# Kernel optimization log

Hardware: AMD Instinct MI355X
Metric: run time of the kernel (lower is better)

The kernel has to match this reference:

```python
import jax, jax.numpy as jnp
import numpy as np

UNITS = 128000
NEGATIVES = 8192
N = 8192
C = 1024


def _log_uniform_expected_count(ids, num_sampled, range_max):
    # log-uniform (Zipfian) sampler: P(c) = (log(c+2)-log(c+1))/log(range_max+1)
    idf = ids.astype(jnp.float32)
    p = (jnp.log(idf + 2.0) - jnp.log(idf + 1.0)) / jnp.log(jnp.float32(range_max + 1.0))
    # unique sampling expected count: E = -expm1(num_sampled * log1p(-p))
    return -jnp.expm1(jnp.float32(num_sampled) * jnp.log1p(-p))


def setup_inputs() -> dict:
    key = jax.random.key(0)
    k1, k2, k3, k4, k5 = jax.random.split(key, 5)
    inputs = jax.random.normal(k1, (N, C), dtype=jnp.float32)
    targets = jax.random.randint(k2, (N,), 0, UNITS, dtype=jnp.int32)
    sampled = jax.random.randint(k3, (NEGATIVES,), 0, UNITS, dtype=jnp.int32)
    kernel = jax.random.normal(k4, (UNITS, C), dtype=jnp.float32) * 0.02
    bias = jax.random.normal(k5, (UNITS,), dtype=jnp.float32) * 0.01
    return {"inputs": inputs, "targets": targets, "sampled": sampled, "kernel": kernel, "bias": bias}


def reference(inputs, targets, sampled, kernel, bias):
    # --- tf.nn.sampled_softmax_loss with log_uniform_candidate_sampler ---
    # gather true class rows: [N, C], [N]
    true_w = kernel[targets]
    true_b = bias[targets]
    # gather sampled class rows: [S, C], [S]
    samp_w = kernel[sampled]
    samp_b = bias[sampled]
    # true logits: [N]
    true_logits = jnp.einsum('nc,nc->n', inputs, true_w) + true_b
    # sampled logits: [N, S]
    samp_logits = jnp.einsum('nc,sc->ns', inputs, samp_w) + samp_b[None, :]
    # remove accidental hits (sampled id == true label)
    acc = sampled[None, :] == targets[:, None]
    samp_logits = jnp.where(acc, samp_logits - 1e9, samp_logits)
    # subtract log expected counts (sampling-probability correction)
    true_logits = true_logits - jnp.log(_log_uniform_expected_count(targets, NEGATIVES, UNITS))
    samp_logits = samp_logits - jnp.log(_log_uniform_expected_count(sampled, NEGATIVES, UNITS))[None, :]
    # softmax CE with the true class at column 0
    out_logits = jnp.concatenate([true_logits[:, None], samp_logits], axis=1)  # [N, 1+S]
    per_example = jax.nn.logsumexp(out_logits, axis=-1) - out_logits[:, 0]
    # loss_reduction='sum_over_batch_size' -> mean
    return jnp.mean(per_example)
```

## Files before the change

kernel.cpp:

```cpp
#include <hip/hip_runtime.h>
#include <cstdint>
#include <cstddef>

#define NUNITS 128000
#define NNEG   8192
#define NROWS  8192
#define NC     1024

typedef unsigned short u16;
typedef float  f32x4  __attribute__((ext_vector_type(4)));
typedef __bf16 bf16x8 __attribute__((ext_vector_type(8)));

__device__ __forceinline__ u16 f2bf(float x) {
    unsigned u = __float_as_uint(x);
    u = (u + 0x7FFFu + ((u >> 16) & 1u)) >> 16;
    return (u16)u;
}

__device__ __forceinline__ float log_expected_count(int id) {
    float idf = (float)id;
    float p = (logf(idf + 2.0f) - logf(idf + 1.0f)) / logf((float)NUNITS + 1.0f);
    float e = -expm1f((float)NNEG * log1pf(-p));
    return logf(e);
}

__global__ void cast_inputs_kernel(const float* __restrict__ in, u16* __restrict__ outp) {
    const int i = blockIdx.x * 256 + threadIdx.x;
    const float4 v = ((const float4*)in)[i];
    ushort4 o;
    o.x = f2bf(v.x); o.y = f2bf(v.y); o.z = f2bf(v.z); o.w = f2bf(v.w);
    ((ushort4*)outp)[i] = o;
}

__global__ void gather_w_kernel(const float* __restrict__ kern, const int* __restrict__ sampled,
                                u16* __restrict__ wout) {
    const int srow = blockIdx.x;
    const int id = sampled[srow];
    const float4* src = (const float4*)(kern + (size_t)id * NC);
    ushort4* dst = (ushort4*)(wout + (size_t)srow * NC);
    const float4 v = src[threadIdx.x];
    ushort4 o;
    o.x = f2bf(v.x); o.y = f2bf(v.y); o.z = f2bf(v.z); o.w = f2bf(v.w);
    dst[threadIdx.x] = o;
}

__global__ void bcorr_kernel(const int* __restrict__ sampled, const float* __restrict__ bias,
                             float* __restrict__ bc) {
    const int i = blockIdx.x * 256 + threadIdx.x;
    const int id = sampled[i];
    bc[i] = bias[id] - log_expected_count(id);
}

__global__ void true_logits_kernel(const float* __restrict__ inputs, const int* __restrict__ targets,
                                   const float* __restrict__ kern, const float* __restrict__ bias,
                                   float* __restrict__ truel) {
    const int wv = threadIdx.x >> 6;
    const int lane = threadIdx.x & 63;
    const int row = blockIdx.x * 4 + wv;
    const int t = targets[row];
    const float4* a = (const float4*)(inputs + (size_t)row * NC);
    const float4* w = (const float4*)(kern + (size_t)t * NC);
    float s = 0.0f;
#pragma unroll
    for (int i = 0; i < 4; ++i) {
        float4 x = a[lane + i * 64];
        float4 y = w[lane + i * 64];
        s += x.x * y.x + x.y * y.y + x.z * y.z + x.w * y.w;
    }
    for (int m = 32; m; m >>= 1) s += __shfl_xor(s, m, 64);
    if (lane == 0) truel[row] = s + bias[t] - log_expected_count(t);
}

__global__ __launch_bounds__(256, 2) void gemm_lse_kernel(
    const u16* __restrict__ Abf, const u16* __restrict__ Wbf,
    const float* __restrict__ bcorr, const int* __restrict__ targets,
    const int* __restrict__ sampled, float* __restrict__ partial) {
    __shared__ u16 lds_A[128 * 32];
    __shared__ u16 lds_W[128 * 32];
    __shared__ int   lds_tgt[128];
    __shared__ int   lds_smp[128];
    __shared__ float lds_bc[128];
    __shared__ float lds_rowsum[128];

    const int tid = threadIdx.x;
    const int wv = tid >> 6;
    const int lane = tid & 63;
    const int bn0 = blockIdx.x * 128;
    const int bm0 = blockIdx.y * 128;
    const int wm = (wv >> 1) * 64;
    const int wn = (wv & 1) * 64;

    if (tid < 128) {
        lds_tgt[tid] = targets[bm0 + tid];
        lds_smp[tid] = sampled[bn0 + tid];
        lds_bc[tid] = bcorr[bn0 + tid];
        lds_rowsum[tid] = 0.0f;
    }

    f32x4 acc[4][4];
    const f32x4 zero4 = {0.0f, 0.0f, 0.0f, 0.0f};
#pragma unroll
    for (int i = 0; i < 4; ++i)
#pragma unroll
        for (int j = 0; j < 4; ++j) acc[i][j] = zero4;

    const int c0 = wv * 2;
    const int rsub = lane >> 2;
    const int cseg = (lane & 3) * 8;
    const int arow = lane & 15;
    const int kq = (lane >> 4) * 8;

    for (int kt = 0; kt < NC / 32; ++kt) {
        const int k0 = kt * 32;
#pragma unroll
        for (int c = 0; c < 2; ++c) {
            const int ch = c0 + c;
            const int rl = ch * 16 + rsub;
            const u16* ga = Abf + (size_t)(bm0 + rl) * NC + k0 + cseg;
            const u16* gw = Wbf + (size_t)(bn0 + rl) * NC + k0 + cseg;
            __builtin_amdgcn_global_load_lds(
                (const __attribute__((address_space(1))) void*)ga,
                (__attribute__((address_space(3))) void*)&lds_A[ch * 512], 16, 0, 0);
            __builtin_amdgcn_global_load_lds(
                (const __attribute__((address_space(1))) void*)gw,
                (__attribute__((address_space(3))) void*)&lds_W[ch * 512], 16, 0, 0);
        }
        __syncthreads();

        bf16x8 af[4], bfv[4];
#pragma unroll
        for (int mt = 0; mt < 4; ++mt)
            af[mt] = *(const bf16x8*)&lds_A[(wm + mt * 16 + arow) * 32 + kq];
#pragma unroll
        for (int nt = 0; nt < 4; ++nt)
            bfv[nt] = *(const bf16x8*)&lds_W[(wn + nt * 16 + arow) * 32 + kq];
#pragma unroll
        for (int mt = 0; mt < 4; ++mt)
#pragma unroll
            for (int nt = 0; nt < 4; ++nt)
                acc[mt][nt] = __builtin_amdgcn_mfma_f32_16x16x32_bf16(
                    af[mt], bfv[nt], acc[mt][nt], 0, 0, 0);
        __syncthreads();
    }

#pragma unroll
    for (int mt = 0; mt < 4; ++mt) {
#pragma unroll
        for (int r = 0; r < 4; ++r) {
            const int row_l = wm + mt * 16 + (lane >> 4) * 4 + r;
            const int tg = lds_tgt[row_l];
            float s = 0.0f;
#pragma unroll
            for (int nt = 0; nt < 4; ++nt) {
                const int col_l = wn + nt * 16 + (lane & 15);
                const float logit = acc[mt][nt][r] + lds_bc[col_l];
                s += (lds_smp[col_l] == tg) ? 0.0f : __expf(logit);
            }
#pragma unroll
            for (int m = 1; m < 16; m <<= 1) s += __shfl_xor(s, m, 64);
            if ((lane & 15) == 0) atomicAdd(&lds_rowsum[row_l], s);
        }
    }
    __syncthreads();
    if (tid < 128) partial[(size_t)(bm0 + tid) * 64 + blockIdx.x] = lds_rowsum[tid];
}

__global__ void row_lse_kernel(const float* __restrict__ partial, const float* __restrict__ truel,
                               float* __restrict__ bsums) {
    const int row = blockIdx.x * 256 + threadIdx.x;
    const float* p = partial + (size_t)row * 64;
    float s = 0.0f;
#pragma unroll
    for (int i = 0; i < 64; ++i) s += p[i];
    const float tl = truel[row];
    float v = logf(s + expf(tl)) - tl;
    for (int m = 32; m; m >>= 1) v += __shfl_xor(v, m, 64);
    __shared__ float red[4];
    if ((threadIdx.x & 63) == 0) red[threadIdx.x >> 6] = v;
    __syncthreads();
    if (threadIdx.x == 0) bsums[blockIdx.x] = red[0] + red[1] + red[2] + red[3];
}

__global__ void finalize_kernel(const float* __restrict__ bsums, float* __restrict__ out) {
    float v = (threadIdx.x < 32) ? bsums[threadIdx.x] : 0.0f;
    for (int m = 32; m; m >>= 1) v += __shfl_xor(v, m, 64);
    if (threadIdx.x == 0) out[0] = v / (float)NROWS;
}

extern "C" void kernel_launch(void* const* d_in, const int* in_sizes, int n_in,
                              void* d_out, int out_size, void* d_ws, size_t ws_size,
                              hipStream_t stream) {
    (void)in_sizes; (void)n_in; (void)out_size; (void)ws_size;
    const float* inputs  = (const float*)d_in[0];
    const int*   targets = (const int*)d_in[1];
    const int*   sampled = (const int*)d_in[2];
    const float* kern    = (const float*)d_in[3];
    const float* bias    = (const float*)d_in[4];
    float* out = (float*)d_out;

    char* ws = (char*)d_ws;
    u16* a_bf = (u16*)ws;
    u16* w_bf = (u16*)(ws + (size_t)16 * 1024 * 1024);
    float* bc    = (float*)(ws + (size_t)32 * 1024 * 1024);
    float* truel = (float*)(ws + (size_t)32 * 1024 * 1024 + 32768);
    float* part  = (float*)(ws + (size_t)32 * 1024 * 1024 + 65536);
    float* bsums = (float*)(ws + (size_t)32 * 1024 * 1024 + 65536 +
                            (size_t)NROWS * 64 * 4);

    cast_inputs_kernel<<<dim3(8192), dim3(256), 0, stream>>>(inputs, a_bf);
    gather_w_kernel<<<dim3(8192), dim3(256), 0, stream>>>(kern, sampled, w_bf);
    bcorr_kernel<<<dim3(32), dim3(256), 0, stream>>>(sampled, bias, bc);
    true_logits_kernel<<<dim3(2048), dim3(256), 0, stream>>>(inputs, targets, kern, bias, truel);
    gemm_lse_kernel<<<dim3(64, 64), dim3(256), 0, stream>>>(a_bf, w_bf, bc, targets, sampled, part);
    row_lse_kernel<<<dim3(32), dim3(256), 0, stream>>>(part, truel, bsums);
    finalize_kernel<<<dim3(1), dim3(64), 0, stream>>>(bsums, out);
}
```

Before: 780.2 us.

## Rewrite fused GEMM-LSE with 256x256 tiles, double-buffered swizzled LDS pipeline

Replaces the 128x128x32 single-buffered GEMM tile with a 256x256x64 tile using 8 waves, double-buffered LDS filled by global_load_lds with an XOR swizzle to avoid bank conflicts. The K loop is split into four MFMA phases interleaved with prefetches of the next tile, using s_setprio and raw barriers. Block IDs are remapped for L2 locality. The aim is more reuse per loaded byte, overlap of loads with MFMA work, and less barrier stall, at the cost of higher register and LDS pressure (64KB of tile buffers).

```diff
diff --git a/kernel.cpp b/kernel.cpp
--- a/kernel.cpp
+++ b/kernel.cpp
@@ -6,6 +6,12 @@
 #define NNEG   8192
 #define NROWS  8192
 #define NC     1024
+
+#define BM 256
+#define BN 256
+#define BK 64
+#define NTK (NC / BK)
+#define SCHUNKS (NNEG / BN)
 
 typedef unsigned short u16;
 typedef float  f32x4  __attribute__((ext_vector_type(4)));
@@ -71,107 +77,203 @@
     if (lane == 0) truel[row] = s + bias[t] - log_expected_count(t);
 }
 
-__global__ __launch_bounds__(256, 2) void gemm_lse_kernel(
+
+#define GLL16(SRC, DST) __builtin_amdgcn_global_load_lds( \
+    (const __attribute__((address_space(1))) void*)(SRC), \
+    (__attribute__((address_space(3))) void*)(DST), 16, 0, 0)
+
+#define MFMA_BF16(A_, B_, C_) __builtin_amdgcn_mfma_f32_16x16x32_bf16((A_), (B_), (C_), 0, 0, 0)
+
+__device__ __forceinline__ void sbar() {
+    __builtin_amdgcn_s_barrier();
+    asm volatile("" ::: "memory");
+}
+
+__global__ __launch_bounds__(512, 2) void gemm_lse_kernel(
     const u16* __restrict__ Abf, const u16* __restrict__ Wbf,
     const float* __restrict__ bcorr, const int* __restrict__ targets,
     const int* __restrict__ sampled, float* __restrict__ partial) {
-    __shared__ u16 lds_A[128 * 32];
-    __shared__ u16 lds_W[128 * 32];
-    __shared__ int   lds_tgt[128];
-    __shared__ int   lds_smp[128];
-    __shared__ float lds_bc[128];
-    __shared__ float lds_rowsum[128];
-
-    const int tid = threadIdx.x;
-    const int wv = tid >> 6;
+    __shared__ u16 lds_A[2][BM * BK];
+    __shared__ u16 lds_B[2][BN * BK];
+    __shared__ int   lds_tgt[BM];
+    __shared__ int   lds_smp[BN];
+    __shared__ float lds_bc[BN];
+    __shared__ float lds_rowsum[BM];
+
+    const int tid  = threadIdx.x;
+    const int wv   = tid >> 6;
     const int lane = tid & 63;
-    const int bn0 = blockIdx.x * 128;
-    const int bm0 = blockIdx.y * 128;
-    const int wm = (wv >> 1) * 64;
-    const int wn = (wv & 1) * 64;
-
-    if (tid < 128) {
+    const int l15  = lane & 15;
+    const int q    = lane >> 4;
+
+    const int bid = blockIdx.x;
+    const int swz = (bid & 7) * (1024 / 8) + (bid >> 3);
+    const int bsx = swz & 31;
+    const int bsy = swz >> 5;
+    const int bm0 = bsy * BM;
+    const int bn0 = bsx * BN;
+
+    const int wmb = (wv >> 2) * 128;
+    const int wnb = (wv & 3) * 64;
+
+    if (tid < 256) {
         lds_tgt[tid] = targets[bm0 + tid];
         lds_smp[tid] = sampled[bn0 + tid];
-        lds_bc[tid] = bcorr[bn0 + tid];
+        lds_bc[tid]  = bcorr[bn0 + tid];
         lds_rowsum[tid] = 0.0f;
     }
 
-    f32x4 acc[4][4];
+    const u16* gA[4]; const u16* gB[4]; int ldsoff[4];
+#pragma unroll
+    for (int i = 0; i < 4; ++i) {
+        const int v  = i * 512 + tid;
+        const int r  = v >> 3;
+        const int gs = (v & 7) ^ (r & 7);
+        gA[i] = Abf + (size_t)(bm0 + r) * NC + gs * 8;
+        gB[i] = Wbf + (size_t)(bn0 + r) * NC + gs * 8;
+        ldsoff[i] = (i * 512 + (wv << 6)) * 8;
+    }
+
+    f32x4 acc[8][4];
     const f32x4 zero4 = {0.0f, 0.0f, 0.0f, 0.0f};
 #pragma unroll
-    for (int i = 0; i < 4; ++i)
-#pragma unroll
-        for (int j = 0; j < 4; ++j) acc[i][j] = zero4;
-
-    const int c0 = wv * 2;
-    const int rsub = lane >> 2;
-    const int cseg = (lane & 3) * 8;
-    const int arow = lane & 15;
-    const int kq = (lane >> 4) * 8;
-
-    for (int kt = 0; kt < NC / 32; ++kt) {
-        const int k0 = kt * 32;
-#pragma unroll
-        for (int c = 0; c < 2; ++c) {
-            const int ch = c0 + c;
-            const int rl = ch * 16 + rsub;
-            const u16* ga = Abf + (size_t)(bm0 + rl) * NC + k0 + cseg;
-            const u16* gw = Wbf + (size_t)(bn0 + rl) * NC + k0 + cseg;
-            __builtin_amdgcn_global_load_lds(
-                (const __attribute__((address_space(1))) void*)ga,
-                (__attribute__((address_space(3))) void*)&lds_A[ch * 512], 16, 0, 0);
-            __builtin_amdgcn_global_load_lds(
-                (const __attribute__((address_space(1))) void*)gw,
-                (__attribute__((address_space(3))) void*)&lds_W[ch * 512], 16, 0, 0);
-        }
-        __syncthreads();
-
-        bf16x8 af[4], bfv[4];
-#pragma unroll
-        for (int mt = 0; mt < 4; ++mt)
-            af[mt] = *(const bf16x8*)&lds_A[(wm + mt * 16 + arow) * 32 + kq];
-#pragma unroll
-        for (int nt = 0; nt < 4; ++nt)
-            bfv[nt] = *(const bf16x8*)&lds_W[(wn + nt * 16 + arow) * 32 + kq];
-#pragma unroll
-        for (int mt = 0; mt < 4; ++mt)
-#pragma unroll
-            for (int nt = 0; nt < 4; ++nt)
-                acc[mt][nt] = __builtin_amdgcn_mfma_f32_16x16x32_bf16(
-                    af[mt], bfv[nt], acc[mt][nt], 0, 0, 0);
-        __syncthreads();
-    }
-
-#pragma unroll
-    for (int mt = 0; mt < 4; ++mt) {
+    for (int m = 0; m < 8; ++m)
+#pragma unroll
+        for (int n = 0; n < 4; ++n) acc[m][n] = zero4;
+
+#pragma unroll
+    for (int i = 0; i < 4; ++i) GLL16(gA[i], &lds_A[0][ldsoff[i]]);
+#pragma unroll
+    for (int i = 0; i < 4; ++i) GLL16(gB[i], &lds_B[0][ldsoff[i]]);
+    __syncthreads();
+
+    const int cb0 = ((q ^ (lane & 7)) << 4);
+
+#pragma unroll 2
+    for (int t = 0; t < NTK; ++t) {
+        const int cur = t & 1;
+        const int nxt = cur ^ 1;
+        const char* lAc = (const char*)lds_A[cur];
+        const char* lBc = (const char*)lds_B[cur];
+        bf16x8 a[4][2], b[4][2];
+
+#pragma unroll
+        for (int m = 0; m < 4; ++m) {
+            const int rb = (wmb + m * 16 + l15) * 128;
+            a[m][0] = *(const bf16x8*)(lAc + rb + cb0);
+            a[m][1] = *(const bf16x8*)(lAc + rb + (cb0 ^ 64));
+        }
+#pragma unroll
+        for (int n = 0; n < 2; ++n) {
+            const int rb = (wnb + n * 16 + l15) * 128;
+            b[n][0] = *(const bf16x8*)(lBc + rb + cb0);
+            b[n][1] = *(const bf16x8*)(lBc + rb + (cb0 ^ 64));
+        }
+        if (t + 1 < NTK) {
+#pragma unroll
+            for (int i = 0; i < 4; ++i) GLL16(gA[i] + (t + 1) * BK, &lds_A[nxt][ldsoff[i]]);
+        }
+        sbar();
+        __builtin_amdgcn_s_setprio(1);
+#pragma unroll
+        for (int m = 0; m < 4; ++m)
+#pragma unroll
+            for (int n = 0; n < 2; ++n) {
+                acc[m][n] = MFMA_BF16(a[m][0], b[n][0], acc[m][n]);
+                acc[m][n] = MFMA_BF16(a[m][1], b[n][1], acc[m][n]);
+            }
+        __builtin_amdgcn_s_setprio(0);
+        sbar();
+
+#pragma unroll
+        for (int n = 0; n < 2; ++n) {
+            const int rb = (wnb + (n + 2) * 16 + l15) * 128;
+            b[n + 2][0] = *(const bf16x8*)(lBc + rb + cb0);
+            b[n + 2][1] = *(const bf16x8*)(lBc + rb + (cb0 ^ 64));
+        }
+        if (t + 1 < NTK) {
+#pragma unroll
+            for (int i = 0; i < 4; ++i) GLL16(gB[i] + (t + 1) * BK, &lds_B[nxt][ldsoff[i]]);
+        }
+        sbar();
+        __builtin_amdgcn_s_setprio(1);
+#pragma unroll
+        for (int m = 0; m < 4; ++m)
+#pragma unroll
+            for (int n = 0; n < 2; ++n) {
+                acc[m][n + 2] = MFMA_BF16(a[m][0], b[n + 2][0], acc[m][n + 2]);
+                acc[m][n + 2] = MFMA_BF16(a[m][1], b[n + 2][1], acc[m][n + 2]);
+            }
+        __builtin_amdgcn_s_setprio(0);
+        sbar();
+
+#pragma unroll
+        for (int m = 0; m < 4; ++m) {
+            const int rb = (wmb + (m + 4) * 16 + l15) * 128;
+            a[m][0] = *(const bf16x8*)(lAc + rb + cb0);
+            a[m][1] = *(const bf16x8*)(lAc + rb + (cb0 ^ 64));
+        }
+        sbar();
+        __builtin_amdgcn_s_setprio(1);
+#pragma unroll
+        for (int m = 0; m < 4; ++m)
+#pragma unroll
+            for (int n = 0; n < 2; ++n) {
+                acc[m + 4][n + 2] = MFMA_BF16(a[m][0], b[n + 2][0], acc[m + 4][n + 2]);
+                acc[m + 4][n + 2] = MFMA_BF16(a[m][1], b[n + 2][1], acc[m + 4][n + 2]);
+            }
+        __builtin_amdgcn_s_setprio(0);
+        sbar();
+
+        __builtin_amdgcn_s_setprio(1);
+#pragma unroll
+        for (int m = 0; m < 4; ++m)
+#pragma unroll
+            for (int n = 0; n < 2; ++n) {
+                acc[m + 4][n] = MFMA_BF16(a[m][0], b[n][0], acc[m + 4][n]);
+                acc[m + 4][n] = MFMA_BF16(a[m][1], b[n][1], acc[m + 4][n]);
+            }
+        __builtin_amdgcn_s_setprio(0);
+        asm volatile("s_waitcnt vmcnt(0)" ::: "memory");
+        __builtin_amdgcn_s_barrier();
+        asm volatile("" ::: "memory");
+    }
+
+    float bcv[4]; int smpv[4];
+#pragma unroll
+    for (int n = 0; n < 4; ++n) {
+        const int c = wnb + n * 16 + l15;
+        bcv[n] = lds_bc[c];
+        smpv[n] = lds_smp[c];
+    }
+#pragma unroll
+    for (int m = 0; m < 8; ++m) {
 #pragma unroll
         for (int r = 0; r < 4; ++r) {
-            const int row_l = wm + mt * 16 + (lane >> 4) * 4 + r;
+            const int row_l = wmb + m * 16 + q * 4 + r;
             const int tg = lds_tgt[row_l];
             float s = 0.0f;
 #pragma unroll
-            for (int nt = 0; nt < 4; ++nt) {
-                const int col_l = wn + nt * 16 + (lane & 15);
-                const float logit = acc[mt][nt][r] + lds_bc[col_l];
-                s += (lds_smp[col_l] == tg) ? 0.0f : __expf(logit);
-            }
-#pragma unroll
-            for (int m = 1; m < 16; m <<= 1) s += __shfl_xor(s, m, 64);
-            if ((lane & 15) == 0) atomicAdd(&lds_rowsum[row_l], s);
+            for (int n = 0; n < 4; ++n) {
+                const float logit = acc[m][n][r] + bcv[n];
+                s += (smpv[n] == tg) ? 0.0f : __expf(logit);
+            }
+#pragma unroll
+            for (int msk = 1; msk < 16; msk <<= 1) s += __shfl_xor(s, msk, 64);
+            if (l15 == 0) atomicAdd(&lds_rowsum[row_l], s);
         }
     }
     __syncthreads();
-    if (tid < 128) partial[(size_t)(bm0 + tid) * 64 + blockIdx.x] = lds_rowsum[tid];
+    if (tid < 256) partial[(size_t)(bm0 + tid) * SCHUNKS + bsx] = lds_rowsum[tid];
 }
 
 __global__ void row_lse_kernel(const float* __restrict__ partial, const float* __restrict__ truel,
                                float* __restrict__ bsums) {
     const int row = blockIdx.x * 256 + threadIdx.x;
-    const float* p = partial + (size_t)row * 64;
+    const float* p = partial + (size_t)row * SCHUNKS;
     float s = 0.0f;
 #pragma unroll
-    for (int i = 0; i < 64; ++i) s += p[i];
+    for (int i = 0; i < SCHUNKS; ++i) s += p[i];
     const float tl = truel[row];
     float v = logf(s + expf(tl)) - tl;
     for (int m = 32; m; m >>= 1) v += __shfl_xor(v, m, 64);
@@ -205,13 +307,13 @@
     float* truel = (float*)(ws + (size_t)32 * 1024 * 1024 + 32768);
     float* part  = (float*)(ws + (size_t)32 * 1024 * 1024 + 65536);
     float* bsums = (float*)(ws + (size_t)32 * 1024 * 1024 + 65536 +
-                            (size_t)NROWS * 64 * 4);
+                            (size_t)NROWS * SCHUNKS * 4);
 
     cast_inputs_kernel<<<dim3(8192), dim3(256), 0, stream>>>(inputs, a_bf);
     gather_w_kernel<<<dim3(8192), dim3(256), 0, stream>>>(kern, sampled, w_bf);
     bcorr_kernel<<<dim3(32), dim3(256), 0, stream>>>(sampled, bias, bc);
     true_logits_kernel<<<dim3(2048), dim3(256), 0, stream>>>(inputs, targets, kern, bias, truel);
-    gemm_lse_kernel<<<dim3(64, 64), dim3(256), 0, stream>>>(a_bf, w_bf, bc, targets, sampled, part);
+    gemm_lse_kernel<<<dim3(1024), dim3(512), 0, stream>>>(a_bf, w_bf, bc, targets, sampled, part);
     row_lse_kernel<<<dim3(32), dim3(256), 0, stream>>>(part, truel, bsums);
     finalize_kernel<<<dim3(1), dim3(64), 0, stream>>>(bsums, out);
 }
```

Measured after the change: 750.4 us. -3.8%, faster.
